# Kernel optimization log

Hardware: AMD Instinct MI355X
Metric: run time of the kernel (lower is better)

Reference implementation:

```python
import jax, jax.numpy as jnp
import numpy as np

D_MODEL = 512
HEADS = 8

def setup_inputs() -> dict:
    key = jax.random.key(0)
    ks = jax.random.split(key, 11)
    B, S, D = 2, 4096, D_MODEL
    s = 1.0 / np.sqrt(D)
    inp = {
        'q': jax.random.normal(ks[0], (B, S, D), jnp.float32),
        'k': jax.random.normal(ks[1], (B, S, D), jnp.float32),
        'v': jax.random.normal(ks[2], (B, S, D), jnp.float32),
        'Wq': jax.random.normal(ks[3], (D, D), jnp.float32) * s,
        'bq': jnp.zeros((D,), jnp.float32),
        'Wk': jax.random.normal(ks[4], (D, D), jnp.float32) * s,
        'bk': jnp.zeros((D,), jnp.float32),
        'Wv': jax.random.normal(ks[5], (D, D), jnp.float32) * s,
        'bv': jnp.zeros((D,), jnp.float32),
        'Wo': jax.random.normal(ks[6], (D, D), jnp.float32) * s,
        'bo': jnp.zeros((D,), jnp.float32),
    }
    return inp

def _split_heads(x, h):
    B, S, D = x.shape
    return x.reshape(B, S, h, D // h).transpose(0, 2, 1, 3)  # [B,H,S,Dh]

def reference(q, k, v, Wq, bq, Wk, bk, Wv, bv, Wo, bo):
    # torch Linear: y = x @ W.T + b
    qh = _split_heads(q @ Wq.T + bq, HEADS)
    kh = _split_heads(k @ Wk.T + bk, HEADS)
    vh = _split_heads(v @ Wv.T + bv, HEADS)
    d_tensor = qh.shape[-1]
    scale = 1.0 / jnp.sqrt(jnp.asarray(d_tensor, qh.dtype))
    score = jnp.einsum('bhqd,bhkd->bhqk', qh, kh) * scale  # [B,H,S,S]
    attn = jax.nn.softmax(score, axis=-1)
    out = jnp.einsum('bhqk,bhkd->bhqd', attn, vh)
    B, H, S, Dh = out.shape
    out = out.transpose(0, 2, 1, 3).reshape(B, S, H * Dh)
    return out @ Wo.T + bo
```

## Files before the change

### kernel.cpp

```cpp
#include <hip/hip_runtime.h>

typedef short bf16x8 __attribute__((ext_vector_type(8)));
typedef float f32x4 __attribute__((ext_vector_type(4)));
typedef float f32x16 __attribute__((ext_vector_type(16)));
typedef unsigned short ushort_t;
typedef unsigned short us8 __attribute__((ext_vector_type(8)));
typedef unsigned short us4 __attribute__((ext_vector_type(4)));
typedef unsigned int u32x4 __attribute__((ext_vector_type(4)));
typedef unsigned int uint2v __attribute__((ext_vector_type(2)));

#define MFMA16(a, b, c) __builtin_amdgcn_mfma_f32_16x16x32_bf16((a), (b), (c), 0, 0, 0)
#define MFMA32(a, b, c) __builtin_amdgcn_mfma_f32_32x32x16_bf16((a), (b), (c), 0, 0, 0)

template <int N> struct ic { static constexpr int value = N; };

static __device__ __forceinline__ ushort_t f2bf(float f) {
    unsigned int u = __builtin_bit_cast(unsigned int, f);
    u += 0x7FFFu + ((u >> 16) & 1u);
    return (ushort_t)(u >> 16);
}

static __device__ __forceinline__ unsigned cvtpk(float lo, float hi) {
    unsigned r;
    asm("v_cvt_pk_bf16_f32 %0, %1, %2" : "=v"(r) : "v"(lo), "v"(hi));
    return r;
}

static __device__ __forceinline__ void gload16(const void* g, void* l) {
    __builtin_amdgcn_global_load_lds(
        (const __attribute__((address_space(1))) unsigned int*)g,
        (__attribute__((address_space(3))) unsigned int*)l,
        16, 0, 0);
}

__global__ __launch_bounds__(256) void cvt_w(const float* __restrict__ W0,
                                             const float* __restrict__ W1,
                                             const float* __restrict__ W2,
                                             const float* __restrict__ W3,
                                             ushort_t* __restrict__ dst) {
    const float* src = (blockIdx.y == 0) ? W0 : (blockIdx.y == 1) ? W1
                     : (blockIdx.y == 2) ? W2 : W3;
    const int i = (blockIdx.x * 256 + threadIdx.x) * 8;
    float4 f0 = *(const float4*)(src + i);
    float4 f1 = *(const float4*)(src + i + 4);
    unsigned tw[4] = {cvtpk(f0.x, f0.y), cvtpk(f0.z, f0.w),
                      cvtpk(f1.x, f1.y), cvtpk(f1.z, f1.w)};
    *(u32x4*)(dst + (size_t)blockIdx.y * 262144 + i) = *(u32x4*)tw;
}

__global__ __launch_bounds__(256) void gemm_qkv(const float* __restrict__ qi,
                                                const float* __restrict__ ki,
                                                const float* __restrict__ vi,
                                                const ushort_t* __restrict__ Wball,
                                                const float* __restrict__ bq,
                                                const float* __restrict__ bk,
                                                const float* __restrict__ bv,
                                                ushort_t* __restrict__ Qh,
                                                ushort_t* __restrict__ Kh,
                                                ushort_t* __restrict__ Vt,
                                                float Cs) {
    constexpr int K = 512;
    __shared__ ushort_t As[64][72];
    __shared__ ushort_t Bs[64][72];

    const int which = blockIdx.y;
    const float*    Ap   = (which == 0) ? qi : (which == 1) ? ki : vi;
    const ushort_t* Wb   = Wball + (size_t)which * 262144;
    const float*    bias = (which == 0) ? bq : (which == 1) ? bk : bv;
    ushort_t*       outp = (which == 0) ? Qh : (which == 1) ? Kh : Vt;

    int bid = blockIdx.x;
    bid = (bid & 7) * 128 + (bid >> 3);
    const int bm = bid >> 3;
    const int bn = bid & 7;
    const int m0 = bm * 64, n0 = bn * 64;
    const int t    = threadIdx.x;
    const int lane = t & 63;
    const int wv   = t >> 6;
    const int wm   = wv >> 1, wn = wv & 1;
    const int lrow = t >> 2;
    const int lcol = (t & 3) * 16;

    const int l15 = lane & 15;
    const int l16 = lane >> 4;

    f32x4 acc[2][2] = {};

    const float*    apf = Ap + (size_t)(m0 + lrow) * K + lcol;
    const ushort_t* bpb = Wb + (size_t)(n0 + lrow) * K + lcol;

    us8 br0, br1;
    f32x4 af[4];

    af[0] = *(const f32x4*)apf;       af[1] = *(const f32x4*)(apf + 4);
    af[2] = *(const f32x4*)(apf + 8); af[3] = *(const f32x4*)(apf + 12);
    br0 = *(const us8*)bpb; br1 = *(const us8*)(bpb + 8);

#pragma unroll 1
    for (int kt = 0; kt < K / 64; ++kt) {
        __syncthreads();
        {
            unsigned tw[8];
#pragma unroll
            for (int i = 0; i < 4; ++i) {
                tw[2 * i]     = cvtpk(af[i][0], af[i][1]);
                tw[2 * i + 1] = cvtpk(af[i][2], af[i][3]);
            }
            *(u32x4*)&As[lrow][lcol]     = *(u32x4*)tw;
            *(u32x4*)&As[lrow][lcol + 8] = *(u32x4*)(tw + 4);
        }
        *(us8*)&Bs[lrow][lcol]     = br0;
        *(us8*)&Bs[lrow][lcol + 8] = br1;
        __syncthreads();

        if (kt < K / 64 - 1) {
            const int off = (kt + 1) * 64;
            const float* s = apf + off;
            af[0] = *(const f32x4*)s;       af[1] = *(const f32x4*)(s + 4);
            af[2] = *(const f32x4*)(s + 8); af[3] = *(const f32x4*)(s + 12);
            br0 = *(const us8*)(bpb + off); br1 = *(const us8*)(bpb + off + 8);
        }

#pragma unroll
        for (int kk = 0; kk < 2; ++kk) {
            bf16x8 a0 = *(const bf16x8*)&As[wm * 32 + l15][kk * 32 + l16 * 8];
            bf16x8 a1 = *(const bf16x8*)&As[wm * 32 + 16 + l15][kk * 32 + l16 * 8];
            bf16x8 b0 = *(const bf16x8*)&Bs[wn * 32 + l15][kk * 32 + l16 * 8];
            bf16x8 b1 = *(const bf16x8*)&Bs[wn * 32 + 16 + l15][kk * 32 + l16 * 8];
            acc[0][0] = MFMA16(a0, b0, acc[0][0]);
            acc[0][1] = MFMA16(a0, b1, acc[0][1]);
            acc[1][0] = MFMA16(a1, b0, acc[1][0]);
            acc[1][1] = MFMA16(a1, b1, acc[1][1]);
        }
    }

#pragma unroll
    for (int i = 0; i < 2; ++i)
#pragma unroll
        for (int j = 0; j < 2; ++j) {
            const int n  = n0 + wn * 32 + j * 16 + l15;
            const float bv_ = bias[n];
            const int h = n >> 6, d = n & 63;
            if (which == 2) {
                const int mbase = m0 + wm * 32 + i * 16 + l16 * 4;
                const int b = mbase >> 12, key = mbase & 4095;
                const int kr = key & 63;
                const int o  = (kr & 7) | ((((kr >> 3) ^ d) & 7) << 3);
                ushort_t tmp[4];
#pragma unroll
                for (int v = 0; v < 4; ++v) tmp[v] = f2bf(acc[i][j][v] + bv_);
                *(us4*)(outp + (size_t)(b * 8 + h) * 262144 +
                        (size_t)(key >> 6) * 4096 + d * 64 + o) = *(us4*)tmp;
            } else if (which == 1) {
#pragma unroll
                for (int v = 0; v < 4; ++v) {
                    const int m = m0 + wm * 32 + i * 16 + l16 * 4 + v;
                    const int b = m >> 12, s = m & 4095;
                    const int row = s & 63;
                    const int o   = (d & 7) | ((((d >> 3) ^ row) & 7) << 3);
                    outp[(size_t)(b * 8 + h) * 262144 + (size_t)(s >> 6) * 4096 +
                         row * 64 + o] = f2bf(acc[i][j][v] + bv_);
                }
            } else {
#pragma unroll
                for (int v = 0; v < 4; ++v) {
                    const int m = m0 + wm * 32 + i * 16 + l16 * 4 + v;
                    const int b = m >> 12, s = m & 4095;
                    outp[(((size_t)(b * 8 + h)) * 4096 + s) * 64 + d] =
                        f2bf((acc[i][j][v] + bv_) * Cs);
                }
            }
        }
}

__global__ __launch_bounds__(256) void gemm_out(const ushort_t* __restrict__ Ap,
                                                const ushort_t* __restrict__ Wb,
                                                const float* __restrict__ bias,
                                                float* __restrict__ outp) {
    constexpr int K = 512;
    __shared__ ushort_t As[64][72];
    __shared__ ushort_t Bs[64][72];

    int bid = blockIdx.x;
    bid = (bid & 7) * 128 + (bid >> 3);
    const int bm = bid >> 3;
    const int bn = bid & 7;
    const int m0 = bm * 64, n0 = bn * 64;
    const int t    = threadIdx.x;
    const int lane = t & 63;
    const int wv   = t >> 6;
    const int wm   = wv >> 1, wn = wv & 1;
    const int lrow = t >> 2;
    const int lcol = (t & 3) * 16;

    const int l15 = lane & 15;
    const int l16 = lane >> 4;

    f32x4 acc[2][2] = {};

    const ushort_t* apb = Ap + (size_t)(m0 + lrow) * K + lcol;
    const ushort_t* bpb = Wb + (size_t)(n0 + lrow) * K + lcol;

    us8 ar0, ar1, br0, br1;
    ar0 = *(const us8*)apb; ar1 = *(const us8*)(apb + 8);
    br0 = *(const us8*)bpb; br1 = *(const us8*)(bpb + 8);

#pragma unroll 1
    for (int kt = 0; kt < K / 64; ++kt) {
        __syncthreads();
        *(us8*)&As[lrow][lcol]     = ar0;
        *(us8*)&As[lrow][lcol + 8] = ar1;
        *(us8*)&Bs[lrow][lcol]     = br0;
        *(us8*)&Bs[lrow][lcol + 8] = br1;
        __syncthreads();

        if (kt < K / 64 - 1) {
            const int off = (kt + 1) * 64;
            ar0 = *(const us8*)(apb + off); ar1 = *(const us8*)(apb + off + 8);
            br0 = *(const us8*)(bpb + off); br1 = *(const us8*)(bpb + off + 8);
        }

#pragma unroll
        for (int kk = 0; kk < 2; ++kk) {
            bf16x8 a0 = *(const bf16x8*)&As[wm * 32 + l15][kk * 32 + l16 * 8];
            bf16x8 a1 = *(const bf16x8*)&As[wm * 32 + 16 + l15][kk * 32 + l16 * 8];
            bf16x8 b0 = *(const bf16x8*)&Bs[wn * 32 + l15][kk * 32 + l16 * 8];
            bf16x8 b1 = *(const bf16x8*)&Bs[wn * 32 + 16 + l15][kk * 32 + l16 * 8];
            acc[0][0] = MFMA16(a0, b0, acc[0][0]);
            acc[0][1] = MFMA16(a0, b1, acc[0][1]);
            acc[1][0] = MFMA16(a1, b0, acc[1][0]);
            acc[1][1] = MFMA16(a1, b1, acc[1][1]);
        }
    }

#pragma unroll
    for (int i = 0; i < 2; ++i)
#pragma unroll
        for (int j = 0; j < 2; ++j) {
            const int n  = n0 + wn * 32 + j * 16 + l15;
            const float bv_ = bias[n];
#pragma unroll
            for (int v = 0; v < 4; ++v) {
                const int m = m0 + wm * 32 + i * 16 + l16 * 4 + v;
                outp[(size_t)m * 512 + n] = acc[i][j][v] + bv_;
            }
        }
}

__global__ __launch_bounds__(256) void attn_fwd(const ushort_t* __restrict__ Qh,
                                                const ushort_t* __restrict__ Kg,
                                                const ushort_t* __restrict__ Vg,
                                                ushort_t* __restrict__ Out) {
    constexpr int S  = 4096;
    constexpr int NT = 64;
    __shared__ __attribute__((aligned(16))) char LDS[32768];

    const int qt = blockIdx.x;
    const int bh = blockIdx.y;
    const int b  = bh >> 3, h = bh & 7;

    const int t    = threadIdx.x;
    const int lane = t & 63;
    const int wv   = t >> 6;
    const int l31  = lane & 31;
    const int hl   = lane >> 5;

    const int qw = qt * 128 + wv * 32;

    bf16x8 qf[4];
    {
        const ushort_t* qp = Qh + ((size_t)bh * S + qw + l31) * 64 + hl * 8;
#pragma unroll
        for (int ds = 0; ds < 4; ++ds) qf[ds] = *(const bf16x8*)(qp + ds * 16);
    }

    const f32x16 fzero = {};
    f32x16 accO[2] = {};
    float ll = 0.f;

    int gofs[4];
#pragma unroll
    for (int j = 0; j < 4; ++j)
        gofs[j] = l31 * 128 + ((j * 32 + hl * 16) ^ ((l31 & 7) << 4));

    const int wvb = wv * 1024;
    const ushort_t* kg = Kg + (size_t)bh * 262144 + wv * 512 + lane * 8;
    const ushort_t* vg = Vg + (size_t)bh * 262144 + wv * 512 + lane * 8;

    auto issue = [&](int kt, auto curc) {
        constexpr int CUR = decltype(curc)::value;
        const ushort_t* kg_ = kg + (size_t)kt * 4096;
        const ushort_t* vg_ = vg + (size_t)kt * 4096;
        gload16(kg_,        LDS + CUR * 8192 + wvb);
        gload16(kg_ + 2048, LDS + CUR * 8192 + 4096 + wvb);
        gload16(vg_,        LDS + 16384 + CUR * 8192 + wvb);
        gload16(vg_ + 2048, LDS + 16384 + CUR * 8192 + 4096 + wvb);
    };

    auto tile = [&](int kt, auto curc) {
        constexpr int CUR = decltype(curc)::value;

        f32x16 sc0, sc1;
        __builtin_amdgcn_s_setprio(1);
        {
            bf16x8 kf = *(const bf16x8*)(LDS + CUR * 8192 + gofs[0]);
            sc0 = MFMA32(kf, qf[0], fzero);
        }
#pragma unroll
        for (int ds = 1; ds < 4; ++ds) {
            bf16x8 kf = *(const bf16x8*)(LDS + CUR * 8192 + gofs[ds]);
            sc0 = MFMA32(kf, qf[ds], sc0);
        }
        {
            bf16x8 kf = *(const bf16x8*)(LDS + CUR * 8192 + 4096 + gofs[0]);
            sc1 = MFMA32(kf, qf[0], fzero);
        }
#pragma unroll
        for (int ds = 1; ds < 4; ++ds) {
            bf16x8 kf = *(const bf16x8*)(LDS + CUR * 8192 + 4096 + gofs[ds]);
            sc1 = MFMA32(kf, qf[ds], sc1);
        }
        __builtin_amdgcn_s_setprio(0);

#pragma unroll
        for (int i = 0; i < 16; ++i) {
            sc0[i] = __builtin_amdgcn_exp2f(sc0[i]);
            sc1[i] = __builtin_amdgcn_exp2f(sc1[i]);
        }

        {
            f32x16 sv = sc0 + sc1;
            float s8[8];
#pragma unroll
            for (int i = 0; i < 8; ++i) s8[i] = sv[i] + sv[i + 8];
            ll += ((s8[0] + s8[1]) + (s8[2] + s8[3])) + ((s8[4] + s8[5]) + (s8[6] + s8[7]));
        }

        bf16x8 pb[4];
#pragma unroll
        for (int ks = 0; ks < 4; ++ks) {
            const int R0 = (ks & 1) * 8;
            float e0, e1, e2, e3, e4, e5, e6, e7;
            if (ks < 2) {
                e0 = sc0[R0+0]; e1 = sc0[R0+1]; e2 = sc0[R0+2]; e3 = sc0[R0+3];
                e4 = sc0[R0+4]; e5 = sc0[R0+5]; e6 = sc0[R0+6]; e7 = sc0[R0+7];
            } else {
                e0 = sc1[R0+0]; e1 = sc1[R0+1]; e2 = sc1[R0+2]; e3 = sc1[R0+3];
                e4 = sc1[R0+4]; e5 = sc1[R0+5]; e6 = sc1[R0+6]; e7 = sc1[R0+7];
            }
            unsigned w0 = cvtpk(e0, e1);
            unsigned w1 = cvtpk(e2, e3);
            unsigned w2 = cvtpk(e4, e5);
            unsigned w3 = cvtpk(e6, e7);
            uint2v s02 = __builtin_amdgcn_permlane32_swap(w0, w2, false, false);
            uint2v s13 = __builtin_amdgcn_permlane32_swap(w1, w3, false, false);
            u32x4 w = {s02.x, s13.x, s02.y, s13.y};
            pb[ks] = __builtin_bit_cast(bf16x8, w);
        }

        __builtin_amdgcn_s_setprio(1);
#pragma unroll
        for (int ks = 0; ks < 4; ++ks) {
            {
                bf16x8 vf = *(const bf16x8*)(LDS + 16384 + CUR * 8192 + gofs[ks]);
                accO[0] = MFMA32(vf, pb[ks], accO[0]);
            }
            {
                bf16x8 vf = *(const bf16x8*)(LDS + 16384 + CUR * 8192 + 4096 + gofs[ks]);
                accO[1] = MFMA32(vf, pb[ks], accO[1]);
            }
        }
        __builtin_amdgcn_s_setprio(0);

        __syncthreads();
        if (kt + 2 < NT) issue(kt + 2, curc);
    };

    issue(0, ic<0>{});
    issue(1, ic<1>{});
    __syncthreads();

#pragma unroll 1
    for (int kt2 = 0; kt2 < NT; kt2 += 2) {
        tile(kt2,     ic<0>{});
        tile(kt2 + 1, ic<1>{});
    }

    const float lt  = ll + __shfl_xor(ll, 32);
    const float inv = 1.0f / lt;
    ushort_t* orow = Out + ((size_t)b * S + qw + l31) * 512 + h * 64;
#pragma unroll
    for (int db = 0; db < 2; ++db)
#pragma unroll
        for (int q4 = 0; q4 < 4; ++q4) {
            unsigned w0 = cvtpk(accO[db][q4 * 4 + 0] * inv, accO[db][q4 * 4 + 1] * inv);
            unsigned w1 = cvtpk(accO[db][q4 * 4 + 2] * inv, accO[db][q4 * 4 + 3] * inv);
            unsigned tmp[2] = {w0, w1};
            *(us4*)(orow + db * 32 + q4 * 8 + hl * 4) = *(const us4*)tmp;
        }
}

extern "C" void kernel_launch(void* const* d_in, const int* in_sizes, int n_in,
                              void* d_out, int out_size, void* d_ws, size_t ws_size,
                              hipStream_t stream) {
    const float* q  = (const float*)d_in[0];
    const float* k  = (const float*)d_in[1];
    const float* v  = (const float*)d_in[2];
    const float* Wq = (const float*)d_in[3];
    const float* bq = (const float*)d_in[4];
    const float* bk = (const float*)d_in[6];
    const float* bv = (const float*)d_in[8];
    const float* bo = (const float*)d_in[10];

    char* w = (char*)d_ws;
    const size_t SZ = (size_t)2 * 8 * 4096 * 64 * 2;

    ushort_t* Qh  = (ushort_t*)(w);
    ushort_t* Kh  = (ushort_t*)(w + SZ);
    ushort_t* Vtr = (ushort_t*)(w + 2 * SZ);
    ushort_t* AO  = (ushort_t*)(w + 3 * SZ);
    ushort_t* Wb  = (ushort_t*)(w + 4 * SZ);

    cvt_w<<<dim3(128, 4), 256, 0, stream>>>(Wq, (const float*)d_in[5],
                                            (const float*)d_in[7], (const float*)d_in[9], Wb);

    const float Cs = 0.125f * 1.44269504f;
    gemm_qkv<<<dim3(1024, 3), 256, 0, stream>>>(q, k, v, Wb, bq, bk, bv, Qh, Kh, Vtr, Cs);

    attn_fwd<<<dim3(32, 16), 256, 0, stream>>>(Qh, Kh, Vtr, AO);

    gemm_out<<<1024, 256, 0, stream>>>(AO, Wb + 3 * 262144, bo, (float*)d_out);
}
```

Baseline: 142.1 us.

## Pre-permute K/V global layout to MFMA fragment order for linear LDS reads

The K and V projection epilogues now write their outputs in a layout already ordered by MFMA fragment (block, k-slice, half, lane, element) instead of an XOR-swizzled row layout. The attention kernel can then read each fragment from LDS at lane*16 plus a constant offset, with no per-lane swizzle arithmetic and without holding the gofs offset registers. The row-sum reduction is also rewritten to use paired float2 adds, aimed at packed FP32 instructions. The change relies on the producer layout and the consumer addressing matching exactly, and linear reads may bring back LDS bank conflicts.

```diff
diff --git a/kernel.cpp b/kernel.cpp
--- a/kernel.cpp
+++ b/kernel.cpp
@@ -1,6 +1,7 @@
 #include <hip/hip_runtime.h>
 
 typedef short bf16x8 __attribute__((ext_vector_type(8)));
+typedef float f32x2 __attribute__((ext_vector_type(2)));
 typedef float f32x4 __attribute__((ext_vector_type(4)));
 typedef float f32x16 __attribute__((ext_vector_type(16)));
 typedef unsigned short ushort_t;
@@ -144,22 +145,25 @@
             if (which == 2) {
                 const int mbase = m0 + wm * 32 + i * 16 + l16 * 4;
                 const int b = mbase >> 12, key = mbase & 4095;
-                const int kr = key & 63;
-                const int o  = (kr & 7) | ((((kr >> 3) ^ d) & 7) << 3);
+                const int keyr = key & 63;
+                const int ks = keyr >> 4, hc = (keyr >> 3) & 1, e0 = keyr & 7;
+                const int db = d >> 5, dr = d & 31;
                 ushort_t tmp[4];
 #pragma unroll
                 for (int v = 0; v < 4; ++v) tmp[v] = f2bf(acc[i][j][v] + bv_);
                 *(us4*)(outp + (size_t)(b * 8 + h) * 262144 +
-                        (size_t)(key >> 6) * 4096 + d * 64 + o) = *(us4*)tmp;
+                        (size_t)(key >> 6) * 4096 +
+                        db * 2048 + ks * 512 + (hc * 32 + dr) * 8 + e0) = *(us4*)tmp;
             } else if (which == 1) {
+                const int jd = d >> 4, hc = (d >> 3) & 1, e = d & 7;
 #pragma unroll
                 for (int v = 0; v < 4; ++v) {
                     const int m = m0 + wm * 32 + i * 16 + l16 * 4 + v;
                     const int b = m >> 12, s = m & 4095;
-                    const int row = s & 63;
-                    const int o   = (d & 7) | ((((d >> 3) ^ row) & 7) << 3);
+                    const int r = s & 63, kb2 = r >> 5, kr = r & 31;
                     outp[(size_t)(b * 8 + h) * 262144 + (size_t)(s >> 6) * 4096 +
-                         row * 64 + o] = f2bf(acc[i][j][v] + bv_);
+                         kb2 * 2048 + jd * 512 + (hc * 32 + kr) * 8 + e] =
+                        f2bf(acc[i][j][v] + bv_);
                 }
             } else {
 #pragma unroll
@@ -278,11 +282,7 @@
     f32x16 accO[2] = {};
     float ll = 0.f;
 
-    int gofs[4];
-#pragma unroll
-    for (int j = 0; j < 4; ++j)
-        gofs[j] = l31 * 128 + ((j * 32 + hl * 16) ^ ((l31 & 7) << 4));
-
+    const char* lbase = LDS + lane * 16;
     const int wvb = wv * 1024;
     const ushort_t* kg = Kg + (size_t)bh * 262144 + wv * 512 + lane * 8;
     const ushort_t* vg = Vg + (size_t)bh * 262144 + wv * 512 + lane * 8;
@@ -303,21 +303,21 @@
         f32x16 sc0, sc1;
         __builtin_amdgcn_s_setprio(1);
         {
-            bf16x8 kf = *(const bf16x8*)(LDS + CUR * 8192 + gofs[0]);
+            bf16x8 kf = *(const bf16x8*)(lbase + CUR * 8192);
             sc0 = MFMA32(kf, qf[0], fzero);
         }
 #pragma unroll
         for (int ds = 1; ds < 4; ++ds) {
-            bf16x8 kf = *(const bf16x8*)(LDS + CUR * 8192 + gofs[ds]);
+            bf16x8 kf = *(const bf16x8*)(lbase + CUR * 8192 + ds * 1024);
             sc0 = MFMA32(kf, qf[ds], sc0);
         }
         {
-            bf16x8 kf = *(const bf16x8*)(LDS + CUR * 8192 + 4096 + gofs[0]);
+            bf16x8 kf = *(const bf16x8*)(lbase + CUR * 8192 + 4096);
             sc1 = MFMA32(kf, qf[0], fzero);
         }
 #pragma unroll
         for (int ds = 1; ds < 4; ++ds) {
-            bf16x8 kf = *(const bf16x8*)(LDS + CUR * 8192 + 4096 + gofs[ds]);
+            bf16x8 kf = *(const bf16x8*)(lbase + CUR * 8192 + 4096 + ds * 1024);
             sc1 = MFMA32(kf, qf[ds], sc1);
         }
         __builtin_amdgcn_s_setprio(0);
@@ -329,11 +329,14 @@
         }
 
         {
-            f32x16 sv = sc0 + sc1;
-            float s8[8];
-#pragma unroll
-            for (int i = 0; i < 8; ++i) s8[i] = sv[i] + sv[i + 8];
-            ll += ((s8[0] + s8[1]) + (s8[2] + s8[3])) + ((s8[4] + s8[5]) + (s8[6] + s8[7]));
+#define PAIR(v, i) __builtin_shufflevector((v), (v), 2 * (i), 2 * (i) + 1)
+            f32x2 pa = (PAIR(sc0, 0) + PAIR(sc0, 1)) + (PAIR(sc0, 2) + PAIR(sc0, 3));
+            f32x2 pbt = (PAIR(sc0, 4) + PAIR(sc0, 5)) + (PAIR(sc0, 6) + PAIR(sc0, 7));
+            f32x2 pc = (PAIR(sc1, 0) + PAIR(sc1, 1)) + (PAIR(sc1, 2) + PAIR(sc1, 3));
+            f32x2 pd = (PAIR(sc1, 4) + PAIR(sc1, 5)) + (PAIR(sc1, 6) + PAIR(sc1, 7));
+            f32x2 s2 = (pa + pbt) + (pc + pd);
+            ll += s2.x + s2.y;
+#undef PAIR
         }
 
         bf16x8 pb[4];
@@ -362,11 +365,11 @@
 #pragma unroll
         for (int ks = 0; ks < 4; ++ks) {
             {
-                bf16x8 vf = *(const bf16x8*)(LDS + 16384 + CUR * 8192 + gofs[ks]);
+                bf16x8 vf = *(const bf16x8*)(lbase + 16384 + CUR * 8192 + ks * 1024);
                 accO[0] = MFMA32(vf, pb[ks], accO[0]);
             }
             {
-                bf16x8 vf = *(const bf16x8*)(LDS + 16384 + CUR * 8192 + 4096 + gofs[ks]);
+                bf16x8 vf = *(const bf16x8*)(lbase + 16384 + CUR * 8192 + 4096 + ks * 1024);
                 accO[1] = MFMA32(vf, pb[ks], accO[1]);
             }
         }
```

After: 140.4 us. No clear change (-1.1%).
